# Kernel optimization log

Measured on AMD Instinct MI355X. Metric: run time of the kernel, lower is better.

Reference implementation:

```python
import jax, jax.numpy as jnp
import numpy as np

B, S, T = 32, 512, 64
DENC = 1024   # encoder dim == dhid
DHID = 1024
DEMB = 512
V = 32000
NEG = 1e20


def setup_inputs() -> dict:
    key = jax.random.key(0)
    ks = jax.random.split(key, 13)
    u = lambda k, shape, a: jax.random.uniform(k, shape, jnp.float32, -a, a)
    klstm = 1.0 / np.sqrt(DHID)
    kproj = 1.0 / np.sqrt(DENC + DHID)
    return {
        "enc": jax.random.normal(ks[0], (B, S, DENC), jnp.float32),
        "inp_mask": jnp.ones((B, S), jnp.float32),
        "label": jax.random.randint(ks[1], (B, T), 0, V),
        "emb_w": jax.random.normal(ks[2], (V, DEMB), jnp.float32) * 0.02,
        "W_ih": u(ks[3], (4 * DHID, DENC + DEMB), klstm),
        "b_ih": u(ks[4], (4 * DHID,), klstm),
        "W_hh": u(ks[5], (4 * DHID, DHID), klstm),
        "b_hh": u(ks[6], (4 * DHID,), klstm),
        "proj_W": u(ks[7], (DEMB, DENC + DHID), kproj),
        "proj_b": u(ks[8], (DEMB,), kproj),
        "emb0": u(ks[9], (DEMB,), 0.1),
        "h0": u(ks[10], (DHID,), 0.1),
        "c0": u(ks[11], (DHID,), 0.1),
    }


def reference(enc, inp_mask, label, emb_w, W_ih, b_ih, W_hh, b_hh,
              proj_W, proj_b, emb0, h0, c0):
    batch = enc.shape[0]
    vocab = emb_w.shape[0]
    h = jnp.broadcast_to(h0, (batch, h0.shape[0]))
    c = jnp.broadcast_to(c0, (batch, c0.shape[0]))
    e = jnp.broadcast_to(emb0, (batch, emb0.shape[0]))
    neg_mask = (1.0 - inp_mask) * NEG  # [B, S]
    emb_T = jax.lax.stop_gradient(emb_w).T  # detached vocab projection

    def step(carry, label_t):
        h, c, e = carry
        # attention over encoder states keyed by h
        score = jnp.einsum('bsd,bd->bs', enc, h) - neg_mask
        attn = jax.nn.softmax(score, axis=1)
        ctx = jnp.einsum('bs,bsd->bd', attn, enc)  # [B, DENC]
        # LSTMCell (torch gate order: i, f, g, o)
        x = jnp.concatenate([ctx, e], axis=1)
        gates = x @ W_ih.T + b_ih + h @ W_hh.T + b_hh
        i, f, g, o = jnp.split(gates, 4, axis=1)
        c = jax.nn.sigmoid(f) * c + jax.nn.sigmoid(i) * jnp.tanh(g)
        h = jax.nn.sigmoid(o) * jnp.tanh(c)
        # project to embedding space, score against vocab
        p = jnp.concatenate([ctx, h], axis=1) @ proj_W.T + proj_b
        out = p @ emb_T  # [B, V]
        # teacher forcing: next input embedding from label
        word = jnp.clip(label_t, 0, vocab - 1)
        e = emb_w[word]
        return (h, c, e), out

    _, outs = jax.lax.scan(step, (h, c, e), label.T)  # outs: [T, B, V]
    return jnp.transpose(outs, (1, 0, 2))  # [B, T, V]
```

## Files before the change

### kernel.cpp

```cpp
#include <hip/hip_runtime.h>
#include <hip/hip_bf16.h>


#define B_   32
#define S_   512
#define T_   64
#define DENC 1024
#define DHID 1024
#define DEMB 512
#define V_   32000
#define KX   2560
#define KP   2048
#define NCH  32

using short8 = __attribute__((ext_vector_type(8))) short;
using f32x4  = __attribute__((ext_vector_type(4))) float;
typedef __hip_bfloat16 bf16;

__device__ __forceinline__ float sigmoidf_(float x) { return 1.0f / (1.0f + expf(-x)); }
__device__ __forceinline__ bf16 bhi(float x) { return __float2bfloat16(x); }
__device__ __forceinline__ bf16 blo(float x) {
    return __float2bfloat16(x - __bfloat162float(__float2bfloat16(x)));
}

#define MFMA(a, b, c) __builtin_amdgcn_mfma_f32_16x16x32_bf16((a), (b), (c), 0, 0, 0)
#define DOT4(a, b) fmaf((a).x, (b).x, fmaf((a).y, (b).y, fmaf((a).z, (b).z, (a).w * (b).w)))


__global__ void k_build_wg(const float* __restrict__ W_ih, const float* __restrict__ W_hh,
                           const float* __restrict__ b_ih, const float* __restrict__ b_hh,
                           bf16* __restrict__ Wh, bf16* __restrict__ Wl, float* __restrict__ bias) {
    int jp = blockIdx.x;
    int g = jp & 3, d = jp >> 2;
    int j = g * 1024 + d;
    const float* wi = W_ih + (size_t)j * 1536;
    const float* wh = W_hh + (size_t)j * 1024;
    bf16* dh = Wh + (size_t)jp * KX;
    bf16* dl = Wl + (size_t)jp * KX;
    for (int i = threadIdx.x; i < 1024; i += 256) { float v = wi[i];      dh[i] = bhi(v);        dl[i] = blo(v); }
    for (int i = threadIdx.x; i < 1024; i += 256) { float v = wh[i];      dh[1024+i] = bhi(v);   dl[1024+i] = blo(v); }
    for (int i = threadIdx.x; i < 512;  i += 256) { float v = wi[1024+i]; dh[2048+i] = bhi(v);   dl[2048+i] = blo(v); }
    if (threadIdx.x == 0) bias[jp] = b_ih[j] + b_hh[j];
}

__global__ void k_cvt(const float* __restrict__ src, bf16* __restrict__ dst, long n) {
    long i = (long)blockIdx.x * blockDim.x + threadIdx.x;
    long stride = (long)gridDim.x * blockDim.x;
    for (; i < n; i += stride) dst[i] = __float2bfloat16(src[i]);
}

__global__ void k_cvt_split(const float* __restrict__ src, bf16* __restrict__ dh,
                            bf16* __restrict__ dl, long n) {
    long i = (long)blockIdx.x * blockDim.x + threadIdx.x;
    long stride = (long)gridDim.x * blockDim.x;
    for (; i < n; i += stride) { float v = src[i]; dh[i] = bhi(v); dl[i] = blo(v); }
}

__global__ void k_init(const float* __restrict__ h0, const float* __restrict__ c0,
                       const float* __restrict__ emb0,
                       float* __restrict__ h, float* __restrict__ c,
                       bf16* __restrict__ Hh, bf16* __restrict__ Hl,
                       bf16* __restrict__ Xh_, bf16* __restrict__ Xl_) {
    int b = blockIdx.x;
    for (int d = threadIdx.x; d < 1024; d += 256) {
        float v = h0[d];
        h[b * 1024 + d] = v;
        c[b * 1024 + d] = c0[d];
        Hh[b * 1024 + d] = bhi(v);
        Hl[b * 1024 + d] = blo(v);
    }
    for (int d = threadIdx.x; d < 512; d += 256) {
        float v = emb0[d];
        Xh_[(size_t)b * KX + 2048 + d] = bhi(v);
        Xl_[(size_t)b * KX + 2048 + d] = blo(v);
    }
}


__global__ __launch_bounds__(256) void k_att(
    const float* __restrict__ enc, const float* __restrict__ mask,
    const float* __restrict__ h,
    bf16* __restrict__ Xh_, bf16* __restrict__ Xl_,
    const bf16* __restrict__ Hh, const bf16* __restrict__ Hl,
    const bf16* __restrict__ PWh, const bf16* __restrict__ PWl,
    const float* __restrict__ pb, const float* __restrict__ emb_w,
    const int* __restrict__ label,
    bf16* __restrict__ Ph, bf16* __restrict__ Pl,
    float* __restrict__ pml, float* __restrict__ pctx, int t)
{
    __shared__ float pr[4][32][17];
    __shared__ float lctx[4][1024];
    __shared__ float lm[4], ll[4];

    int bid = blockIdx.x;
    int tid = threadIdx.x, wave = tid >> 6, lane = tid & 63;

    if (bid < 32) {
        if (t == 0) return;
        int tp = t - 1;
        int nb = bid * 16;
        int ncol = nb + (lane & 15);
        int kc = wave * 512;
        const short* ah;
        const short* al;
        size_t astr, aoff;
        if (wave < 2) { ah = (const short*)Xh_; al = (const short*)Xl_; astr = KX;   aoff = kc; }
        else          { ah = (const short*)Hh;  al = (const short*)Hl;  astr = 1024; aoff = kc - 1024; }
        const short* wrh = (const short*)PWh + (size_t)ncol * KP + kc + (lane >> 4) * 8;
        const short* wrl = (const short*)PWl + (size_t)ncol * KP + kc + (lane >> 4) * 8;
        size_t arow0 = (size_t)(lane & 15) * astr + aoff + (lane >> 4) * 8;
        size_t arow1 = (size_t)((lane & 15) + 16) * astr + aoff + (lane >> 4) * 8;
        f32x4 acc0 = {0, 0, 0, 0}, acc1 = {0, 0, 0, 0};
#pragma unroll 4
        for (int kk = 0; kk < 16; ++kk) {
            int ko = kk * 32;
            short8 a0h = *(const short8*)(ah + arow0 + ko);
            short8 a1h = *(const short8*)(ah + arow1 + ko);
            short8 a0l = *(const short8*)(al + arow0 + ko);
            short8 a1l = *(const short8*)(al + arow1 + ko);
            short8 bh = *(const short8*)(wrh + ko);
            short8 bl = *(const short8*)(wrl + ko);
            acc0 = MFMA(a0h, bh, acc0); acc1 = MFMA(a1h, bh, acc1);
            acc0 = MFMA(a0h, bl, acc0); acc1 = MFMA(a1h, bl, acc1);
            acc0 = MFMA(a0l, bh, acc0); acc1 = MFMA(a1l, bh, acc1);
        }
#pragma unroll
        for (int r = 0; r < 4; ++r) {
            pr[wave][(lane >> 4) * 4 + r][lane & 15]      = acc0[r];
            pr[wave][16 + (lane >> 4) * 4 + r][lane & 15] = acc1[r];
        }
        __syncthreads();
        for (int p = tid; p < 512; p += 256) {
            int bb = p >> 4, col = p & 15;
            float v = pr[0][bb][col] + pr[1][bb][col] + pr[2][bb][col] + pr[3][bb][col]
                      + pb[nb + col];
            size_t mi = (size_t)(bb * 64 + tp) * 512 + nb + col;
            Ph[mi] = bhi(v);
            Pl[mi] = blo(v);
        }
        int b = bid;
        int wd = label[b * 64 + tp];
        wd = wd < 0 ? 0 : (wd > V_ - 1 ? V_ - 1 : wd);
        const float* ew = emb_w + (size_t)wd * 512;
        for (int d = tid; d < 512; d += 256) {
            float v = ew[d];
            Xh_[(size_t)b * KX + 2048 + d] = bhi(v);
            Xl_[(size_t)b * KX + 2048 + d] = blo(v);
        }
        return;
    }

    if (t >= T_) return;
    int ab = bid - 32;
    int b = ab >> 5, ch = ab & (NCH - 1);

    float4 hreg[4];
    const float4* h4p = (const float4*)(h + b * 1024);
#pragma unroll
    for (int j = 0; j < 4; ++j) hreg[j] = h4p[j * 64 + lane];

    const float* encb = enc + (size_t)b * S_ * DENC;
    int srow0 = ch * 16 + wave * 4;
    const float4* r0 = (const float4*)(encb + (size_t)(srow0 + 0) * DENC);
    const float4* r1 = (const float4*)(encb + (size_t)(srow0 + 1) * DENC);
    const float4* r2 = (const float4*)(encb + (size_t)(srow0 + 2) * DENC);
    const float4* r3 = (const float4*)(encb + (size_t)(srow0 + 3) * DENC);
    float4 e00 = r0[lane], e01 = r0[64+lane], e02 = r0[128+lane], e03 = r0[192+lane];
    float4 e10 = r1[lane], e11 = r1[64+lane], e12 = r1[128+lane], e13 = r1[192+lane];
    float4 e20 = r2[lane], e21 = r2[64+lane], e22 = r2[128+lane], e23 = r2[192+lane];
    float4 e30 = r3[lane], e31 = r3[64+lane], e32 = r3[128+lane], e33 = r3[192+lane];

    float d0 = DOT4(e00,hreg[0]) + DOT4(e01,hreg[1]) + DOT4(e02,hreg[2]) + DOT4(e03,hreg[3]);
    float d1 = DOT4(e10,hreg[0]) + DOT4(e11,hreg[1]) + DOT4(e12,hreg[2]) + DOT4(e13,hreg[3]);
    float d2 = DOT4(e20,hreg[0]) + DOT4(e21,hreg[1]) + DOT4(e22,hreg[2]) + DOT4(e23,hreg[3]);
    float d3 = DOT4(e30,hreg[0]) + DOT4(e31,hreg[1]) + DOT4(e32,hreg[2]) + DOT4(e33,hreg[3]);
#pragma unroll
    for (int off = 32; off; off >>= 1) {
        d0 += __shfl_xor(d0, off, 64);
        d1 += __shfl_xor(d1, off, 64);
        d2 += __shfl_xor(d2, off, 64);
        d3 += __shfl_xor(d3, off, 64);
    }
    float sc0 = d0 - (1.0f - mask[b * S_ + srow0 + 0]) * 1e20f;
    float sc1 = d1 - (1.0f - mask[b * S_ + srow0 + 1]) * 1e20f;
    float sc2 = d2 - (1.0f - mask[b * S_ + srow0 + 2]) * 1e20f;
    float sc3 = d3 - (1.0f - mask[b * S_ + srow0 + 3]) * 1e20f;
    float mw = fmaxf(fmaxf(sc0, sc1), fmaxf(sc2, sc3));
    float w0 = expf(sc0 - mw), w1 = expf(sc1 - mw);
    float w2 = expf(sc2 - mw), w3 = expf(sc3 - mw);
    float lw = w0 + w1 + w2 + w3;
    float4 c0, c1, c2, c3;
    c0.x = w0*e00.x + w1*e10.x + w2*e20.x + w3*e30.x;
    c0.y = w0*e00.y + w1*e10.y + w2*e20.y + w3*e30.y;
    c0.z = w0*e00.z + w1*e10.z + w2*e20.z + w3*e30.z;
    c0.w = w0*e00.w + w1*e10.w + w2*e20.w + w3*e30.w;
    c1.x = w0*e01.x + w1*e11.x + w2*e21.x + w3*e31.x;
    c1.y = w0*e01.y + w1*e11.y + w2*e21.y + w3*e31.y;
    c1.z = w0*e01.z + w1*e11.z + w2*e21.z + w3*e31.z;
    c1.w = w0*e01.w + w1*e11.w + w2*e21.w + w3*e31.w;
    c2.x = w0*e02.x + w1*e12.x + w2*e22.x + w3*e32.x;
    c2.y = w0*e02.y + w1*e12.y + w2*e22.y + w3*e32.y;
    c2.z = w0*e02.z + w1*e12.z + w2*e22.z + w3*e32.z;
    c2.w = w0*e02.w + w1*e12.w + w2*e22.w + w3*e32.w;
    c3.x = w0*e03.x + w1*e13.x + w2*e23.x + w3*e33.x;
    c3.y = w0*e03.y + w1*e13.y + w2*e23.y + w3*e33.y;
    c3.z = w0*e03.z + w1*e13.z + w2*e23.z + w3*e33.z;
    c3.w = w0*e03.w + w1*e13.w + w2*e23.w + w3*e33.w;

    ((float4*)lctx[wave])[0 * 64 + lane] = c0;
    ((float4*)lctx[wave])[1 * 64 + lane] = c1;
    ((float4*)lctx[wave])[2 * 64 + lane] = c2;
    ((float4*)lctx[wave])[3 * 64 + lane] = c3;
    if (lane == 0) { lm[wave] = mw; ll[wave] = lw; }
    __syncthreads();

    float mb_ = fmaxf(fmaxf(lm[0], lm[1]), fmaxf(lm[2], lm[3]));
    float q0 = expf(lm[0] - mb_), q1 = expf(lm[1] - mb_);
    float q2 = expf(lm[2] - mb_), q3 = expf(lm[3] - mb_);
    float lb = ll[0] * q0 + ll[1] * q1 + ll[2] * q2 + ll[3] * q3;
    float4 a0 = ((float4*)lctx[0])[tid], a1 = ((float4*)lctx[1])[tid];
    float4 a2 = ((float4*)lctx[2])[tid], a3 = ((float4*)lctx[3])[tid];
    float4 v;
    v.x = a0.x * q0 + a1.x * q1 + a2.x * q2 + a3.x * q3;
    v.y = a0.y * q0 + a1.y * q1 + a2.y * q2 + a3.y * q3;
    v.z = a0.z * q0 + a1.z * q1 + a2.z * q2 + a3.z * q3;
    v.w = a0.w * q0 + a1.w * q1 + a2.w * q2 + a3.w * q3;
    int pi = b * NCH + ch;
    ((float4*)(pctx + (size_t)pi * 1024))[tid] = v;
    if (tid == 0) { pml[pi * 2] = mb_; pml[pi * 2 + 1] = lb; }
}


__global__ __launch_bounds__(256) void k_comb(const float* __restrict__ pml,
                                              const float* __restrict__ pctx,
                                              const bf16* __restrict__ Hh,
                                              const bf16* __restrict__ Hl,
                                              bf16* __restrict__ Xh_, bf16* __restrict__ Xl_) {
    __shared__ float sml[NCH * 2];
    __shared__ float wch[NCH];
    int b = blockIdx.x, tid = threadIdx.x;
    if (tid < NCH * 2) sml[tid] = pml[b * NCH * 2 + tid];
    __syncthreads();
    float mf = -3.0e38f;
#pragma unroll
    for (int c = 0; c < NCH; ++c) mf = fmaxf(mf, sml[2 * c]);
    float lt = 0.f;
#pragma unroll
    for (int c = 0; c < NCH; ++c) lt += sml[2 * c + 1] * expf(sml[2 * c] - mf);
    if (tid < NCH) wch[tid] = expf(sml[2 * tid] - mf);
    __syncthreads();
    float inv = 1.0f / lt;
    const float4* base = (const float4*)(pctx + (size_t)b * NCH * 1024) + tid;
    float4 sacc = {0, 0, 0, 0};
#pragma unroll 8
    for (int c = 0; c < NCH; ++c) {
        float wc = wch[c];
        float4 p = base[c * 256];
        sacc.x = fmaf(wc, p.x, sacc.x); sacc.y = fmaf(wc, p.y, sacc.y);
        sacc.z = fmaf(wc, p.z, sacc.z); sacc.w = fmaf(wc, p.w, sacc.w);
    }
    sacc.x *= inv; sacc.y *= inv; sacc.z *= inv; sacc.w *= inv;
    size_t xi = (size_t)b * KX + tid * 4;
    Xh_[xi + 0] = bhi(sacc.x); Xl_[xi + 0] = blo(sacc.x);
    Xh_[xi + 1] = bhi(sacc.y); Xl_[xi + 1] = blo(sacc.y);
    Xh_[xi + 2] = bhi(sacc.z); Xl_[xi + 2] = blo(sacc.z);
    Xh_[xi + 3] = bhi(sacc.w); Xl_[xi + 3] = blo(sacc.w);
    ((unsigned long long*)(Xh_ + (size_t)b * KX + 1024))[tid] =
        ((const unsigned long long*)(Hh + (size_t)b * 1024))[tid];
    ((unsigned long long*)(Xl_ + (size_t)b * KX + 1024))[tid] =
        ((const unsigned long long*)(Hl + (size_t)b * 1024))[tid];
}


__global__ __launch_bounds__(256) void k_gates(
    const bf16* __restrict__ Xh_, const bf16* __restrict__ Xl_,
    const bf16* __restrict__ Wh_, const bf16* __restrict__ Wl_,
    const float* __restrict__ bias,
    float* __restrict__ c, float* __restrict__ h,
    bf16* __restrict__ Hh, bf16* __restrict__ Hl)
{
    __shared__ float pr[4][32][17];
    int jb = blockIdx.x * 16;
    int tid = threadIdx.x, wave = tid >> 6, lane = tid & 63;
    int jcol = jb + (lane & 15);
    int kc = wave * 640 + (lane >> 4) * 8;
    const short* xhp = (const short*)Xh_ + kc;
    const short* xlp = (const short*)Xl_ + kc;
    const short* wrh = (const short*)Wh_ + (size_t)jcol * KX + kc;
    const short* wrl = (const short*)Wl_ + (size_t)jcol * KX + kc;
    size_t arow0 = (size_t)(lane & 15) * KX;
    size_t arow1 = (size_t)((lane & 15) + 16) * KX;
    f32x4 acc0 = {0, 0, 0, 0}, acc1 = {0, 0, 0, 0};
#pragma unroll 4
    for (int kk = 0; kk < 20; ++kk) {
        int ko = kk * 32;
        short8 a0h = *(const short8*)(xhp + arow0 + ko);
        short8 a1h = *(const short8*)(xhp + arow1 + ko);
        short8 a0l = *(const short8*)(xlp + arow0 + ko);
        short8 a1l = *(const short8*)(xlp + arow1 + ko);
        short8 bh = *(const short8*)(wrh + ko);
        short8 bl = *(const short8*)(wrl + ko);
        acc0 = MFMA(a0h, bh, acc0); acc1 = MFMA(a1h, bh, acc1);
        acc0 = MFMA(a0h, bl, acc0); acc1 = MFMA(a1h, bl, acc1);
        acc0 = MFMA(a0l, bh, acc0); acc1 = MFMA(a1l, bh, acc1);
    }
#pragma unroll
    for (int r = 0; r < 4; ++r) {
        pr[wave][(lane >> 4) * 4 + r][lane & 15]      = acc0[r];
        pr[wave][16 + (lane >> 4) * 4 + r][lane & 15] = acc1[r];
    }
    __syncthreads();
    if (tid < 128) {
        int bb = tid & 31, dd = tid >> 5;
        int cb = dd * 4;
        float gi = pr[0][bb][cb+0] + pr[1][bb][cb+0] + pr[2][bb][cb+0] + pr[3][bb][cb+0] + bias[jb+cb+0];
        float gf = pr[0][bb][cb+1] + pr[1][bb][cb+1] + pr[2][bb][cb+1] + pr[3][bb][cb+1] + bias[jb+cb+1];
        float gg = pr[0][bb][cb+2] + pr[1][bb][cb+2] + pr[2][bb][cb+2] + pr[3][bb][cb+2] + bias[jb+cb+2];
        float go = pr[0][bb][cb+3] + pr[1][bb][cb+3] + pr[2][bb][cb+3] + pr[3][bb][cb+3] + bias[jb+cb+3];
        int d = (jb >> 2) + dd;
        float cv = c[bb * 1024 + d];
        float cn = sigmoidf_(gf) * cv + sigmoidf_(gi) * tanhf(gg);
        float hn = sigmoidf_(go) * tanhf(cn);
        c[bb * 1024 + d] = cn;
        h[bb * 1024 + d] = hn;
        Hh[bb * 1024 + d] = bhi(hn);
        Hl[bb * 1024 + d] = blo(hn);
    }
}


__global__ __launch_bounds__(256) void k_out(const bf16* __restrict__ Ph,
                                             const bf16* __restrict__ Pl,
                                             const bf16* __restrict__ Eb,
                                             float* __restrict__ out) {
    int bid = blockIdx.x;
    int xcd = bid & 7, idx = bid >> 3;
    int vb_grp = xcd * 63 + (idx >> 5);
    if (vb_grp >= 500) return;
    int vb = vb_grp * 64;
    int mb = (idx & 31) * 64;

    __shared__ __align__(16) short ps[64][268];
    int tid = threadIdx.x, wave = tid >> 6, lane = tid & 63;
    int wr = (wave >> 1) * 32, wc = (wave & 1) * 32;
    f32x4 acc[2][2] = {{{0, 0, 0, 0}, {0, 0, 0, 0}}, {{0, 0, 0, 0}, {0, 0, 0, 0}}};
    const short* e0p = (const short*)Eb + (size_t)(vb + wc + (lane & 15)) * 512 + (lane >> 4) * 8;
    const short* e1p = e0p + 16 * 512;
    int srow = tid >> 5, scol = (tid & 31) * 8;

    short8 sr[8];
#pragma unroll
    for (int j = 0; j < 8; ++j)
        sr[j] = *(const short8*)((const short*)Ph + (size_t)(mb + srow + j * 8) * 512 + scol);

    short8 br0[8], br1[8];
    for (int ph = 0; ph < 4; ++ph) {
        int q = ph >> 1;
        if ((ph & 1) == 0) {
#pragma unroll
            for (int kk = 0; kk < 8; ++kk) {
                br0[kk] = *(const short8*)(e0p + q * 256 + kk * 32);
                br1[kk] = *(const short8*)(e1p + q * 256 + kk * 32);
            }
        }
        __syncthreads();
#pragma unroll
        for (int j = 0; j < 8; ++j)
            *(short8*)&ps[srow + j * 8][scol] = sr[j];
        __syncthreads();
        if (ph < 3) {
            int nq = (ph + 1) >> 1;
            const short* nsrc = ((ph + 1) & 1) ? (const short*)Pl : (const short*)Ph;
#pragma unroll
            for (int j = 0; j < 8; ++j)
                sr[j] = *(const short8*)(nsrc + (size_t)(mb + srow + j * 8) * 512 + nq * 256 + scol);
        }
#pragma unroll
        for (int kk = 0; kk < 8; ++kk) {
            int kcol = kk * 32 + (lane >> 4) * 8;
            short8 a0 = *(const short8*)(&ps[wr + (lane & 15)][kcol]);
            short8 a1 = *(const short8*)(&ps[wr + 16 + (lane & 15)][kcol]);
            acc[0][0] = MFMA(a0, br0[kk], acc[0][0]);
            acc[0][1] = MFMA(a0, br1[kk], acc[0][1]);
            acc[1][0] = MFMA(a1, br0[kk], acc[1][0]);
            acc[1][1] = MFMA(a1, br1[kk], acc[1][1]);
        }
    }
#pragma unroll
    for (int f0 = 0; f0 < 2; ++f0)
#pragma unroll
        for (int f1 = 0; f1 < 2; ++f1)
#pragma unroll
            for (int r = 0; r < 4; ++r) {
                int mm = mb + wr + 16 * f0 + (lane >> 4) * 4 + r;
                int vv = vb + wc + 16 * f1 + (lane & 15);
                __builtin_nontemporal_store(acc[f0][f1][r], &out[(size_t)mm * V_ + vv]);
            }
}


extern "C" void kernel_launch(void* const* d_in, const int* in_sizes, int n_in,
                              void* d_out, int out_size, void* d_ws, size_t ws_size,
                              hipStream_t stream) {
    (void)in_sizes; (void)n_in; (void)out_size; (void)ws_size;
    const float* enc    = (const float*)d_in[0];
    const float* mask   = (const float*)d_in[1];
    const int*   label  = (const int*)d_in[2];
    const float* emb_w  = (const float*)d_in[3];
    const float* W_ih   = (const float*)d_in[4];
    const float* b_ih   = (const float*)d_in[5];
    const float* W_hh   = (const float*)d_in[6];
    const float* b_hh   = (const float*)d_in[7];
    const float* proj_W = (const float*)d_in[8];
    const float* proj_b = (const float*)d_in[9];
    const float* emb0   = (const float*)d_in[10];
    const float* h0     = (const float*)d_in[11];
    const float* c0     = (const float*)d_in[12];
    float* out = (float*)d_out;

    char* w = (char*)d_ws;
    size_t o = 0;
    bf16* Wgh  = (bf16*)(w + o); o += (size_t)4096 * KX * 2;
    bf16* Wgl  = (bf16*)(w + o); o += (size_t)4096 * KX * 2;
    bf16* PWh  = (bf16*)(w + o); o += (size_t)512 * KP * 2;
    bf16* PWl  = (bf16*)(w + o); o += (size_t)512 * KP * 2;
    bf16* Eb   = (bf16*)(w + o); o += (size_t)V_ * 512 * 2;
    float* bias= (float*)(w + o); o += 4096 * 4;
    bf16* Xh   = (bf16*)(w + o); o += (size_t)32 * KX * 2;
    bf16* Xl   = (bf16*)(w + o); o += (size_t)32 * KX * 2;
    bf16* Hh   = (bf16*)(w + o); o += (size_t)32 * 1024 * 2;
    bf16* Hl   = (bf16*)(w + o); o += (size_t)32 * 1024 * 2;
    bf16* Ph   = (bf16*)(w + o); o += (size_t)2048 * 512 * 2;
    bf16* Pl   = (bf16*)(w + o); o += (size_t)2048 * 512 * 2;
    float* hb  = (float*)(w + o); o += (size_t)32 * 1024 * 4;
    float* cb  = (float*)(w + o); o += (size_t)32 * 1024 * 4;
    float* pml = (float*)(w + o); o += (size_t)32 * NCH * 2 * 4;
    float* pctx= (float*)(w + o); o += (size_t)32 * NCH * 1024 * 4;

    k_build_wg<<<4096, 256, 0, stream>>>(W_ih, W_hh, b_ih, b_hh, Wgh, Wgl, bias);
    k_cvt_split<<<1024, 256, 0, stream>>>(proj_W, PWh, PWl, (long)512 * KP);
    k_cvt<<<8192, 256, 0, stream>>>(emb_w, Eb, (long)V_ * 512);
    k_init<<<32, 256, 0, stream>>>(h0, c0, emb0, hb, cb, Hh, Hl, Xh, Xl);

    for (int t = 0; t <= T_; ++t) {
        k_att<<<32 + 32 * NCH, 256, 0, stream>>>(enc, mask, hb, Xh, Xl, Hh, Hl,
                                                 PWh, PWl, proj_b, emb_w, label,
                                                 Ph, Pl, pml, pctx, t);
        if (t < T_) {
            k_comb<<<32, 256, 0, stream>>>(pml, pctx, Hh, Hl, Xh, Xl);
            k_gates<<<256, 256, 0, stream>>>(Xh, Xl, Wgh, Wgl, bias, cb, hb, Hh, Hl);
        }
    }
    k_out<<<16128, 256, 0, stream>>>(Ph, Pl, Eb, out);
}
```

Baseline: 3.497 ms.

## Fuse recurrent timestep loop into one cooperative persistent kernel with grid syncs

Replaces the per-timestep launches of attention, combine and gates kernels with a single cooperative kernel that loops over timesteps and uses grid.sync between phases. X and H are double-buffered so the projection of step t-1 can run alongside the combine of step t. A multi-kernel fallback is kept in case the cooperative launch fails. The output GEMM kernel is also rewritten: the XCD-aware block mapping and register prefetch are dropped in favour of staging the hi and lo P tiles in shared memory, with embedding rows read directly from global memory. This trades launch overhead for grid-wide barrier cost and lower occupancy per phase, with 512 blocks each doing two attention units.

```diff
diff --git a/kernel.cpp b/kernel.cpp
--- a/kernel.cpp
+++ b/kernel.cpp
@@ -1,5 +1,8 @@
 #include <hip/hip_runtime.h>
 #include <hip/hip_bf16.h>
+#include <hip/hip_cooperative_groups.h>
+
+namespace cg = cooperative_groups;
 
 
 #define B_   32
@@ -59,100 +62,32 @@
 __global__ void k_init(const float* __restrict__ h0, const float* __restrict__ c0,
                        const float* __restrict__ emb0,
                        float* __restrict__ h, float* __restrict__ c,
-                       bf16* __restrict__ Hh, bf16* __restrict__ Hl,
-                       bf16* __restrict__ Xh_, bf16* __restrict__ Xl_) {
+                       bf16* __restrict__ H0h, bf16* __restrict__ H0l,
+                       bf16* __restrict__ X0h, bf16* __restrict__ X0l) {
     int b = blockIdx.x;
     for (int d = threadIdx.x; d < 1024; d += 256) {
         float v = h0[d];
         h[b * 1024 + d] = v;
         c[b * 1024 + d] = c0[d];
-        Hh[b * 1024 + d] = bhi(v);
-        Hl[b * 1024 + d] = blo(v);
+        H0h[b * 1024 + d] = bhi(v);
+        H0l[b * 1024 + d] = blo(v);
     }
     for (int d = threadIdx.x; d < 512; d += 256) {
         float v = emb0[d];
-        Xh_[(size_t)b * KX + 2048 + d] = bhi(v);
-        Xl_[(size_t)b * KX + 2048 + d] = blo(v);
-    }
-}
-
-
-__global__ __launch_bounds__(256) void k_att(
+        X0h[(size_t)b * KX + 2048 + d] = bhi(v);
+        X0l[(size_t)b * KX + 2048 + d] = blo(v);
+    }
+}
+
+
+__device__ __forceinline__ void att_unit(
     const float* __restrict__ enc, const float* __restrict__ mask,
     const float* __restrict__ h,
-    bf16* __restrict__ Xh_, bf16* __restrict__ Xl_,
-    const bf16* __restrict__ Hh, const bf16* __restrict__ Hl,
-    const bf16* __restrict__ PWh, const bf16* __restrict__ PWl,
-    const float* __restrict__ pb, const float* __restrict__ emb_w,
-    const int* __restrict__ label,
-    bf16* __restrict__ Ph, bf16* __restrict__ Pl,
-    float* __restrict__ pml, float* __restrict__ pctx, int t)
-{
-    __shared__ float pr[4][32][17];
+    float* __restrict__ pml, float* __restrict__ pctx, int b, int ch)
+{
     __shared__ float lctx[4][1024];
     __shared__ float lm[4], ll[4];
-
-    int bid = blockIdx.x;
     int tid = threadIdx.x, wave = tid >> 6, lane = tid & 63;
-
-    if (bid < 32) {
-        if (t == 0) return;
-        int tp = t - 1;
-        int nb = bid * 16;
-        int ncol = nb + (lane & 15);
-        int kc = wave * 512;
-        const short* ah;
-        const short* al;
-        size_t astr, aoff;
-        if (wave < 2) { ah = (const short*)Xh_; al = (const short*)Xl_; astr = KX;   aoff = kc; }
-        else          { ah = (const short*)Hh;  al = (const short*)Hl;  astr = 1024; aoff = kc - 1024; }
-        const short* wrh = (const short*)PWh + (size_t)ncol * KP + kc + (lane >> 4) * 8;
-        const short* wrl = (const short*)PWl + (size_t)ncol * KP + kc + (lane >> 4) * 8;
-        size_t arow0 = (size_t)(lane & 15) * astr + aoff + (lane >> 4) * 8;
-        size_t arow1 = (size_t)((lane & 15) + 16) * astr + aoff + (lane >> 4) * 8;
-        f32x4 acc0 = {0, 0, 0, 0}, acc1 = {0, 0, 0, 0};
-#pragma unroll 4
-        for (int kk = 0; kk < 16; ++kk) {
-            int ko = kk * 32;
-            short8 a0h = *(const short8*)(ah + arow0 + ko);
-            short8 a1h = *(const short8*)(ah + arow1 + ko);
-            short8 a0l = *(const short8*)(al + arow0 + ko);
-            short8 a1l = *(const short8*)(al + arow1 + ko);
-            short8 bh = *(const short8*)(wrh + ko);
-            short8 bl = *(const short8*)(wrl + ko);
-            acc0 = MFMA(a0h, bh, acc0); acc1 = MFMA(a1h, bh, acc1);
-            acc0 = MFMA(a0h, bl, acc0); acc1 = MFMA(a1h, bl, acc1);
-            acc0 = MFMA(a0l, bh, acc0); acc1 = MFMA(a1l, bh, acc1);
-        }
-#pragma unroll
-        for (int r = 0; r < 4; ++r) {
-            pr[wave][(lane >> 4) * 4 + r][lane & 15]      = acc0[r];
-            pr[wave][16 + (lane >> 4) * 4 + r][lane & 15] = acc1[r];
-        }
-        __syncthreads();
-        for (int p = tid; p < 512; p += 256) {
-            int bb = p >> 4, col = p & 15;
-            float v = pr[0][bb][col] + pr[1][bb][col] + pr[2][bb][col] + pr[3][bb][col]
-                      + pb[nb + col];
-            size_t mi = (size_t)(bb * 64 + tp) * 512 + nb + col;
-            Ph[mi] = bhi(v);
-            Pl[mi] = blo(v);
-        }
-        int b = bid;
-        int wd = label[b * 64 + tp];
-        wd = wd < 0 ? 0 : (wd > V_ - 1 ? V_ - 1 : wd);
-        const float* ew = emb_w + (size_t)wd * 512;
-        for (int d = tid; d < 512; d += 256) {
-            float v = ew[d];
-            Xh_[(size_t)b * KX + 2048 + d] = bhi(v);
-            Xl_[(size_t)b * KX + 2048 + d] = blo(v);
-        }
-        return;
-    }
-
-    if (t >= T_) return;
-    int ab = bid - 32;
-    int b = ab >> 5, ch = ab & (NCH - 1);
 
     float4 hreg[4];
     const float4* h4p = (const float4*)(h + b * 1024);
@@ -228,17 +163,17 @@
     int pi = b * NCH + ch;
     ((float4*)(pctx + (size_t)pi * 1024))[tid] = v;
     if (tid == 0) { pml[pi * 2] = mb_; pml[pi * 2 + 1] = lb; }
-}
-
-
-__global__ __launch_bounds__(256) void k_comb(const float* __restrict__ pml,
-                                              const float* __restrict__ pctx,
-                                              const bf16* __restrict__ Hh,
-                                              const bf16* __restrict__ Hl,
-                                              bf16* __restrict__ Xh_, bf16* __restrict__ Xl_) {
+    __syncthreads();
+}
+
+__device__ __forceinline__ void comb_fn(
+    const float* __restrict__ pml, const float* __restrict__ pctx,
+    const bf16* __restrict__ Hth, const bf16* __restrict__ Htl,
+    bf16* __restrict__ Xch, bf16* __restrict__ Xcl, int b)
+{
     __shared__ float sml[NCH * 2];
     __shared__ float wch[NCH];
-    int b = blockIdx.x, tid = threadIdx.x;
+    int tid = threadIdx.x;
     if (tid < NCH * 2) sml[tid] = pml[b * NCH * 2 + tid];
     __syncthreads();
     float mf = -3.0e38f;
@@ -261,26 +196,90 @@
     }
     sacc.x *= inv; sacc.y *= inv; sacc.z *= inv; sacc.w *= inv;
     size_t xi = (size_t)b * KX + tid * 4;
-    Xh_[xi + 0] = bhi(sacc.x); Xl_[xi + 0] = blo(sacc.x);
-    Xh_[xi + 1] = bhi(sacc.y); Xl_[xi + 1] = blo(sacc.y);
-    Xh_[xi + 2] = bhi(sacc.z); Xl_[xi + 2] = blo(sacc.z);
-    Xh_[xi + 3] = bhi(sacc.w); Xl_[xi + 3] = blo(sacc.w);
-    ((unsigned long long*)(Xh_ + (size_t)b * KX + 1024))[tid] =
-        ((const unsigned long long*)(Hh + (size_t)b * 1024))[tid];
-    ((unsigned long long*)(Xl_ + (size_t)b * KX + 1024))[tid] =
-        ((const unsigned long long*)(Hl + (size_t)b * 1024))[tid];
-}
-
-
-__global__ __launch_bounds__(256) void k_gates(
+    Xch[xi + 0] = bhi(sacc.x); Xcl[xi + 0] = blo(sacc.x);
+    Xch[xi + 1] = bhi(sacc.y); Xcl[xi + 1] = blo(sacc.y);
+    Xch[xi + 2] = bhi(sacc.z); Xcl[xi + 2] = blo(sacc.z);
+    Xch[xi + 3] = bhi(sacc.w); Xcl[xi + 3] = blo(sacc.w);
+    ((unsigned long long*)(Xch + (size_t)b * KX + 1024))[tid] =
+        ((const unsigned long long*)(Hth + (size_t)b * 1024))[tid];
+    ((unsigned long long*)(Xcl + (size_t)b * KX + 1024))[tid] =
+        ((const unsigned long long*)(Htl + (size_t)b * 1024))[tid];
+    __syncthreads();
+}
+
+__device__ __forceinline__ void proj_fn(
+    const bf16* __restrict__ Xph, const bf16* __restrict__ Xpl,
+    const bf16* __restrict__ Hph, const bf16* __restrict__ Hpl,
+    const bf16* __restrict__ PWh, const bf16* __restrict__ PWl,
+    const float* __restrict__ pb, const float* __restrict__ emb_w,
+    const int* __restrict__ label,
+    bf16* __restrict__ Ph, bf16* __restrict__ Pl,
+    bf16* __restrict__ Xeh, bf16* __restrict__ Xel,
+    int nbBlk, int tp)
+{
+    __shared__ float pr[4][32][17];
+    int tid = threadIdx.x, wave = tid >> 6, lane = tid & 63;
+    int nb = nbBlk * 16;
+    int ncol = nb + (lane & 15);
+    int kc = wave * 512;
+    const short* ah;
+    const short* al;
+    size_t astr, aoff;
+    if (wave < 2) { ah = (const short*)Xph; al = (const short*)Xpl; astr = KX;   aoff = kc; }
+    else          { ah = (const short*)Hph; al = (const short*)Hpl; astr = 1024; aoff = kc - 1024; }
+    const short* wrh = (const short*)PWh + (size_t)ncol * KP + kc + (lane >> 4) * 8;
+    const short* wrl = (const short*)PWl + (size_t)ncol * KP + kc + (lane >> 4) * 8;
+    size_t arow0 = (size_t)(lane & 15) * astr + aoff + (lane >> 4) * 8;
+    size_t arow1 = (size_t)((lane & 15) + 16) * astr + aoff + (lane >> 4) * 8;
+    f32x4 acc0 = {0, 0, 0, 0}, acc1 = {0, 0, 0, 0};
+#pragma unroll 4
+    for (int kk = 0; kk < 16; ++kk) {
+        int ko = kk * 32;
+        short8 a0h = *(const short8*)(ah + arow0 + ko);
+        short8 a1h = *(const short8*)(ah + arow1 + ko);
+        short8 a0l = *(const short8*)(al + arow0 + ko);
+        short8 a1l = *(const short8*)(al + arow1 + ko);
+        short8 bh = *(const short8*)(wrh + ko);
+        short8 bl = *(const short8*)(wrl + ko);
+        acc0 = MFMA(a0h, bh, acc0); acc1 = MFMA(a1h, bh, acc1);
+        acc0 = MFMA(a0h, bl, acc0); acc1 = MFMA(a1h, bl, acc1);
+        acc0 = MFMA(a0l, bh, acc0); acc1 = MFMA(a1l, bh, acc1);
+    }
+#pragma unroll
+    for (int r = 0; r < 4; ++r) {
+        pr[wave][(lane >> 4) * 4 + r][lane & 15]      = acc0[r];
+        pr[wave][16 + (lane >> 4) * 4 + r][lane & 15] = acc1[r];
+    }
+    __syncthreads();
+    for (int p = tid; p < 512; p += 256) {
+        int bb = p >> 4, col = p & 15;
+        float v = pr[0][bb][col] + pr[1][bb][col] + pr[2][bb][col] + pr[3][bb][col]
+                  + pb[nb + col];
+        size_t mi = (size_t)(bb * 64 + tp) * 512 + nb + col;
+        Ph[mi] = bhi(v);
+        Pl[mi] = blo(v);
+    }
+    int b = nbBlk;
+    int wd = label[b * 64 + tp];
+    wd = wd < 0 ? 0 : (wd > V_ - 1 ? V_ - 1 : wd);
+    const float* ew = emb_w + (size_t)wd * 512;
+    for (int d = tid; d < 512; d += 256) {
+        float v = ew[d];
+        Xeh[(size_t)b * KX + 2048 + d] = bhi(v);
+        Xel[(size_t)b * KX + 2048 + d] = blo(v);
+    }
+    __syncthreads();
+}
+
+__device__ __forceinline__ void gates_fn(
     const bf16* __restrict__ Xh_, const bf16* __restrict__ Xl_,
     const bf16* __restrict__ Wh_, const bf16* __restrict__ Wl_,
     const float* __restrict__ bias,
     float* __restrict__ c, float* __restrict__ h,
-    bf16* __restrict__ Hh, bf16* __restrict__ Hl)
-{
-    __shared__ float pr[4][32][17];
-    int jb = blockIdx.x * 16;
+    bf16* __restrict__ Hnh, bf16* __restrict__ Hnl, int jbBlk)
+{
+    __shared__ float pr2[4][32][17];
+    int jb = jbBlk * 16;
     int tid = threadIdx.x, wave = tid >> 6, lane = tid & 63;
     int jcol = jb + (lane & 15);
     int kc = wave * 640 + (lane >> 4) * 8;
@@ -306,26 +305,117 @@
     }
 #pragma unroll
     for (int r = 0; r < 4; ++r) {
-        pr[wave][(lane >> 4) * 4 + r][lane & 15]      = acc0[r];
-        pr[wave][16 + (lane >> 4) * 4 + r][lane & 15] = acc1[r];
+        pr2[wave][(lane >> 4) * 4 + r][lane & 15]      = acc0[r];
+        pr2[wave][16 + (lane >> 4) * 4 + r][lane & 15] = acc1[r];
     }
     __syncthreads();
     if (tid < 128) {
         int bb = tid & 31, dd = tid >> 5;
-        int cb = dd * 4;
-        float gi = pr[0][bb][cb+0] + pr[1][bb][cb+0] + pr[2][bb][cb+0] + pr[3][bb][cb+0] + bias[jb+cb+0];
-        float gf = pr[0][bb][cb+1] + pr[1][bb][cb+1] + pr[2][bb][cb+1] + pr[3][bb][cb+1] + bias[jb+cb+1];
-        float gg = pr[0][bb][cb+2] + pr[1][bb][cb+2] + pr[2][bb][cb+2] + pr[3][bb][cb+2] + bias[jb+cb+2];
-        float go = pr[0][bb][cb+3] + pr[1][bb][cb+3] + pr[2][bb][cb+3] + pr[3][bb][cb+3] + bias[jb+cb+3];
+        int cb2 = dd * 4;
+        float gi = pr2[0][bb][cb2+0] + pr2[1][bb][cb2+0] + pr2[2][bb][cb2+0] + pr2[3][bb][cb2+0] + bias[jb+cb2+0];
+        float gf = pr2[0][bb][cb2+1] + pr2[1][bb][cb2+1] + pr2[2][bb][cb2+1] + pr2[3][bb][cb2+1] + bias[jb+cb2+1];
+        float gg = pr2[0][bb][cb2+2] + pr2[1][bb][cb2+2] + pr2[2][bb][cb2+2] + pr2[3][bb][cb2+2] + bias[jb+cb2+2];
+        float go = pr2[0][bb][cb2+3] + pr2[1][bb][cb2+3] + pr2[2][bb][cb2+3] + pr2[3][bb][cb2+3] + bias[jb+cb2+3];
         int d = (jb >> 2) + dd;
         float cv = c[bb * 1024 + d];
         float cn = sigmoidf_(gf) * cv + sigmoidf_(gi) * tanhf(gg);
         float hn = sigmoidf_(go) * tanhf(cn);
         c[bb * 1024 + d] = cn;
         h[bb * 1024 + d] = hn;
-        Hh[bb * 1024 + d] = bhi(hn);
-        Hl[bb * 1024 + d] = blo(hn);
-    }
+        Hnh[bb * 1024 + d] = bhi(hn);
+        Hnl[bb * 1024 + d] = blo(hn);
+    }
+    __syncthreads();
+}
+
+
+__global__ __launch_bounds__(256, 2) void k_loop(
+    const float* enc, const float* mask, const int* label, const float* emb_w,
+    const bf16* PWh, const bf16* PWl, const float* pb,
+    const bf16* Wgh, const bf16* Wgl, const float* bias,
+    float* hb, float* cb,
+    bf16* X0h, bf16* X0l, bf16* X1h, bf16* X1l,
+    bf16* H0h, bf16* H0l, bf16* H1h, bf16* H1l,
+    bf16* Ph, bf16* Pl, float* pml, float* pctx)
+{
+    cg::grid_group grid = cg::this_grid();
+    int bid = blockIdx.x;
+
+    for (int t = 0; t <= T_; ++t) {
+        int p = t & 1;
+        bf16* Xch = p ? X1h : X0h;
+        bf16* Xcl = p ? X1l : X0l;
+        const bf16* Xph = p ? X0h : X1h;
+        const bf16* Xpl = p ? X0l : X1l;
+        const bf16* Hth = p ? H1h : H0h;
+        const bf16* Htl = p ? H1l : H0l;
+        bf16* Hnh = p ? H0h : H1h;
+        bf16* Hnl = p ? H0l : H1l;
+
+        if (t < T_) {
+            att_unit(enc, mask, hb, pml, pctx, (bid * 2) >> 5, (bid * 2) & 31);
+            att_unit(enc, mask, hb, pml, pctx, (bid * 2 + 1) >> 5, (bid * 2 + 1) & 31);
+            grid.sync();
+        }
+        if (bid < 32) {
+            if (t < T_) comb_fn(pml, pctx, Hth, Htl, Xch, Xcl, bid);
+        } else if (bid < 64 && t >= 1) {
+            proj_fn(Xph, Xpl, Hth, Htl, PWh, PWl, pb, emb_w, label,
+                    Ph, Pl, Xch, Xcl, bid - 32, t - 1);
+        }
+        if (t < T_) {
+            grid.sync();
+            if (bid < 256)
+                gates_fn(Xch, Xcl, Wgh, Wgl, bias, cb, hb, Hnh, Hnl, bid);
+            grid.sync();
+        }
+    }
+}
+
+
+__global__ __launch_bounds__(256) void k_attw(
+    const float* enc, const float* mask, const float* hb,
+    float* pml, float* pctx)
+{
+    int unit = blockIdx.x;
+    att_unit(enc, mask, hb, pml, pctx, unit >> 5, unit & 31);
+}
+
+__global__ __launch_bounds__(256) void k_cpw(
+    const int* label, const float* emb_w,
+    const bf16* PWh, const bf16* PWl, const float* pb,
+    bf16* X0h, bf16* X0l, bf16* X1h, bf16* X1l,
+    bf16* H0h, bf16* H0l, bf16* H1h, bf16* H1l,
+    bf16* Ph, bf16* Pl, float* pml, float* pctx, int t)
+{
+    int p = t & 1;
+    bf16* Xch = p ? X1h : X0h;
+    bf16* Xcl = p ? X1l : X0l;
+    const bf16* Xph = p ? X0h : X1h;
+    const bf16* Xpl = p ? X0l : X1l;
+    const bf16* Hth = p ? H1h : H0h;
+    const bf16* Htl = p ? H1l : H0l;
+    int bid = blockIdx.x;
+    if (bid < 32) {
+        if (t < T_) comb_fn(pml, pctx, Hth, Htl, Xch, Xcl, bid);
+    } else if (t >= 1) {
+        proj_fn(Xph, Xpl, Hth, Htl, PWh, PWl, pb, emb_w, label,
+                Ph, Pl, Xch, Xcl, bid - 32, t - 1);
+    }
+}
+
+__global__ __launch_bounds__(256) void k_gatesw(
+    const bf16* Wgh, const bf16* Wgl, const float* bias,
+    float* cb, float* hb,
+    bf16* X0h, bf16* X0l, bf16* X1h, bf16* X1l,
+    bf16* H0h, bf16* H0l, bf16* H1h, bf16* H1l, int t)
+{
+    int p = t & 1;
+    const bf16* Xch = p ? X1h : X0h;
+    const bf16* Xcl = p ? X1l : X0l;
+    bf16* Hnh = p ? H0h : H1h;
+    bf16* Hnl = p ? H0l : H1l;
+    gates_fn(Xch, Xcl, Wgh, Wgl, bias, cb, hb, Hnh, Hnl, blockIdx.x);
 }
 
 
@@ -334,56 +424,41 @@
                                              const bf16* __restrict__ Eb,
                                              float* __restrict__ out) {
     int bid = blockIdx.x;
-    int xcd = bid & 7, idx = bid >> 3;
-    int vb_grp = xcd * 63 + (idx >> 5);
-    if (vb_grp >= 500) return;
-    int vb = vb_grp * 64;
-    int mb = (idx & 31) * 64;
-
-    __shared__ __align__(16) short ps[64][268];
+    int vb = (bid >> 5) * 64;
+    int mb = (bid & 31) * 64;
+    __shared__ __align__(16) short ph[64][264];
+    __shared__ __align__(16) short pl[64][264];
     int tid = threadIdx.x, wave = tid >> 6, lane = tid & 63;
     int wr = (wave >> 1) * 32, wc = (wave & 1) * 32;
     f32x4 acc[2][2] = {{{0, 0, 0, 0}, {0, 0, 0, 0}}, {{0, 0, 0, 0}, {0, 0, 0, 0}}};
-    const short* e0p = (const short*)Eb + (size_t)(vb + wc + (lane & 15)) * 512 + (lane >> 4) * 8;
-    const short* e1p = e0p + 16 * 512;
-    int srow = tid >> 5, scol = (tid & 31) * 8;
-
-    short8 sr[8];
-#pragma unroll
-    for (int j = 0; j < 8; ++j)
-        sr[j] = *(const short8*)((const short*)Ph + (size_t)(mb + srow + j * 8) * 512 + scol);
-
-    short8 br0[8], br1[8];
-    for (int ph = 0; ph < 4; ++ph) {
-        int q = ph >> 1;
-        if ((ph & 1) == 0) {
-#pragma unroll
-            for (int kk = 0; kk < 8; ++kk) {
-                br0[kk] = *(const short8*)(e0p + q * 256 + kk * 32);
-                br1[kk] = *(const short8*)(e1p + q * 256 + kk * 32);
-            }
+    const short* e0 = (const short*)Eb + (size_t)(vb + wc + (lane & 15)) * 512 + (lane >> 4) * 8;
+    const short* e1 = e0 + 16 * 512;
+
+    for (int q = 0; q < 2; ++q) {
+        __syncthreads();
+        for (int i = tid; i < 64 * 32; i += 256) {
+            int r = i >> 5, cc = i & 31;
+            ((short8*)&ph[r][0])[cc] = *(const short8*)((const short*)Ph + (size_t)(mb + r) * 512 + q * 256 + cc * 8);
+            ((short8*)&pl[r][0])[cc] = *(const short8*)((const short*)Pl + (size_t)(mb + r) * 512 + q * 256 + cc * 8);
         }
         __syncthreads();
 #pragma unroll
-        for (int j = 0; j < 8; ++j)
-            *(short8*)&ps[srow + j * 8][scol] = sr[j];
-        __syncthreads();
-        if (ph < 3) {
-            int nq = (ph + 1) >> 1;
-            const short* nsrc = ((ph + 1) & 1) ? (const short*)Pl : (const short*)Ph;
-#pragma unroll
-            for (int j = 0; j < 8; ++j)
-                sr[j] = *(const short8*)(nsrc + (size_t)(mb + srow + j * 8) * 512 + nq * 256 + scol);
-        }
-#pragma unroll
         for (int kk = 0; kk < 8; ++kk) {
             int kcol = kk * 32 + (lane >> 4) * 8;
-            short8 a0 = *(const short8*)(&ps[wr + (lane & 15)][kcol]);
-            short8 a1 = *(const short8*)(&ps[wr + 16 + (lane & 15)][kcol]);
-            acc[0][0] = MFMA(a0, br0[kk], acc[0][0]);
-            acc[0][1] = MFMA(a0, br1[kk], acc[0][1]);
-            acc[1][0] = MFMA(a1, br0[kk], acc[1][0]);
-            acc[1][1] = MFMA(a1, br1[kk], acc[1][1]);
+            short8 a0h = *(const short8*)(&ph[wr + (lane & 15)][kcol]);
+            short8 a1h = *(const short8*)(&ph[wr + 16 + (lane & 15)][kcol]);
+            short8 a0l = *(const short8*)(&pl[wr + (lane & 15)][kcol]);
+            short8 a1l = *(const short8*)(&pl[wr + 16 + (lane & 15)][kcol]);
+            short8 b0 = *(const short8*)(e0 + q * 256 + kk * 32);
+            short8 b1 = *(const short8*)(e1 + q * 256 + kk * 32);
+            acc[0][0] = MFMA(a0h, b0, acc[0][0]);
+            acc[0][1] = MFMA(a0h, b1, acc[0][1]);
+            acc[1][0] = MFMA(a1h, b0, acc[1][0]);
+            acc[1][1] = MFMA(a1h, b1, acc[1][1]);
+            acc[0][0] = MFMA(a0l, b0, acc[0][0]);
+            acc[0][1] = MFMA(a0l, b1, acc[0][1]);
+            acc[1][0] = MFMA(a1l, b0, acc[1][0]);
+            acc[1][1] = MFMA(a1l, b1, acc[1][1]);
         }
     }
 #pragma unroll
@@ -426,10 +501,14 @@
     bf16* PWl  = (bf16*)(w + o); o += (size_t)512 * KP * 2;
     bf16* Eb   = (bf16*)(w + o); o += (size_t)V_ * 512 * 2;
     float* bias= (float*)(w + o); o += 4096 * 4;
-    bf16* Xh   = (bf16*)(w + o); o += (size_t)32 * KX * 2;
-    bf16* Xl   = (bf16*)(w + o); o += (size_t)32 * KX * 2;
-    bf16* Hh   = (bf16*)(w + o); o += (size_t)32 * 1024 * 2;
-    bf16* Hl   = (bf16*)(w + o); o += (size_t)32 * 1024 * 2;
+    bf16* X0h  = (bf16*)(w + o); o += (size_t)32 * KX * 2;
+    bf16* X0l  = (bf16*)(w + o); o += (size_t)32 * KX * 2;
+    bf16* X1h  = (bf16*)(w + o); o += (size_t)32 * KX * 2;
+    bf16* X1l  = (bf16*)(w + o); o += (size_t)32 * KX * 2;
+    bf16* H0h  = (bf16*)(w + o); o += (size_t)32 * 1024 * 2;
+    bf16* H0l  = (bf16*)(w + o); o += (size_t)32 * 1024 * 2;
+    bf16* H1h  = (bf16*)(w + o); o += (size_t)32 * 1024 * 2;
+    bf16* H1l  = (bf16*)(w + o); o += (size_t)32 * 1024 * 2;
     bf16* Ph   = (bf16*)(w + o); o += (size_t)2048 * 512 * 2;
     bf16* Pl   = (bf16*)(w + o); o += (size_t)2048 * 512 * 2;
     float* hb  = (float*)(w + o); o += (size_t)32 * 1024 * 4;
@@ -440,16 +519,31 @@
     k_build_wg<<<4096, 256, 0, stream>>>(W_ih, W_hh, b_ih, b_hh, Wgh, Wgl, bias);
     k_cvt_split<<<1024, 256, 0, stream>>>(proj_W, PWh, PWl, (long)512 * KP);
     k_cvt<<<8192, 256, 0, stream>>>(emb_w, Eb, (long)V_ * 512);
-    k_init<<<32, 256, 0, stream>>>(h0, c0, emb0, hb, cb, Hh, Hl, Xh, Xl);
-
-    for (int t = 0; t <= T_; ++t) {
-        k_att<<<32 + 32 * NCH, 256, 0, stream>>>(enc, mask, hb, Xh, Xl, Hh, Hl,
-                                                 PWh, PWl, proj_b, emb_w, label,
-                                                 Ph, Pl, pml, pctx, t);
-        if (t < T_) {
-            k_comb<<<32, 256, 0, stream>>>(pml, pctx, Hh, Hl, Xh, Xl);
-            k_gates<<<256, 256, 0, stream>>>(Xh, Xl, Wgh, Wgl, bias, cb, hb, Hh, Hl);
+    k_init<<<32, 256, 0, stream>>>(h0, c0, emb0, hb, cb, H0h, H0l, X0h, X0l);
+
+    void* kargs[] = {
+        (void*)&enc, (void*)&mask, (void*)&label, (void*)&emb_w,
+        (void*)&PWh, (void*)&PWl, (void*)&proj_b,
+        (void*)&Wgh, (void*)&Wgl, (void*)&bias,
+        (void*)&hb, (void*)&cb,
+        (void*)&X0h, (void*)&X0l, (void*)&X1h, (void*)&X1l,
+        (void*)&H0h, (void*)&H0l, (void*)&H1h, (void*)&H1l,
+        (void*)&Ph, (void*)&Pl, (void*)&pml, (void*)&pctx };
+    hipError_t cerr = hipLaunchCooperativeKernel((void*)k_loop, dim3(512), dim3(256),
+                                                 kargs, 0u, stream);
+    if (cerr != hipSuccess) {
+        for (int t = 0; t <= T_; ++t) {
+            if (t < T_)
+                k_attw<<<1024, 256, 0, stream>>>(enc, mask, hb, pml, pctx);
+            k_cpw<<<64, 256, 0, stream>>>(label, emb_w, PWh, PWl, proj_b,
+                                          X0h, X0l, X1h, X1l,
+                                          H0h, H0l, H1h, H1l,
+                                          Ph, Pl, pml, pctx, t);
+            if (t < T_)
+                k_gatesw<<<256, 256, 0, stream>>>(Wgh, Wgl, bias, cb, hb,
+                                                  X0h, X0l, X1h, X1l,
+                                                  H0h, H0l, H1h, H1l, t);
         }
     }
-    k_out<<<16128, 256, 0, stream>>>(Ph, Pl, Eb, out);
-}
+    k_out<<<16000, 256, 0, stream>>>(Ph, Pl, Eb, out);
+}
```

Result: slower. 13.62 ms (+289.6%).
